# Performance work log

Hardware: AMD Instinct MI355X
Metric: run time of the kernel (lower is better)

## Reference

```python
import jax, jax.numpy as jnp
import numpy as np

B, S, W = 32, 256, 32
T = 16               # topics per doc, each spanning L = S//T sentences
VOCAB, E, H, D = 400001, 300, 128, 128


def _gru_scan(x, Wih, Whh, bih, bhh, reverse=False):
    """x: [B,S,E] -> (outputs [B,S,H], final hidden [B,H]). Torch GRU cell math."""
    h0 = jnp.zeros((x.shape[0], Whh.shape[1]), x.dtype)
    gi_all = jnp.einsum('bse,ge->bsg', x, Wih) + bih  # precompute input gates [B,S,3H]

    def step(h, gi):
        gh = h @ Whh.T + bhh
        ir, iz, inn = jnp.split(gi, 3, axis=-1)
        hr, hz, hn = jnp.split(gh, 3, axis=-1)
        r = jax.nn.sigmoid(ir + hr)
        z = jax.nn.sigmoid(iz + hz)
        n = jnp.tanh(inn + r * hn)
        h_new = (1.0 - z) * n + z * h
        return h_new, h_new

    hT, hs = jax.lax.scan(step, h0, jnp.swapaxes(gi_all, 0, 1), reverse=reverse)
    return jnp.swapaxes(hs, 0, 1), hT


def setup_inputs() -> dict:
    key = jax.random.key(0)
    ks = jax.random.split(key, 16)
    sc_i = 1.0 / np.sqrt(H)
    L = S // T
    starts = (jnp.arange(T, dtype=jnp.int32) * L + 1)          # 1-based inclusive
    ends = (jnp.arange(T, dtype=jnp.int32) + 1) * L
    tse = jnp.broadcast_to(jnp.stack([starts, ends], axis=-1)[None], (B, T, 2)).astype(jnp.int32)
    return {
        'word_ids': jax.random.randint(ks[0], (B, S, W), 0, VOCAB, dtype=jnp.int32),
        'topic_start_ends': tse,
        'embed_table': jax.random.normal(ks[1], (VOCAB, E), jnp.float32) * 0.6,
        'Wih_f': jax.random.normal(ks[2], (3 * H, E), jnp.float32) * sc_i,
        'Whh_f': jax.random.normal(ks[3], (3 * H, H), jnp.float32) * sc_i,
        'bih_f': jax.random.normal(ks[4], (3 * H,), jnp.float32) * sc_i,
        'bhh_f': jax.random.normal(ks[5], (3 * H,), jnp.float32) * sc_i,
        'Wih_b': jax.random.normal(ks[6], (3 * H, E), jnp.float32) * sc_i,
        'Whh_b': jax.random.normal(ks[7], (3 * H, H), jnp.float32) * sc_i,
        'bih_b': jax.random.normal(ks[8], (3 * H,), jnp.float32) * sc_i,
        'bhh_b': jax.random.normal(ks[9], (3 * H,), jnp.float32) * sc_i,
        'v_attention': jax.random.normal(ks[10], (4 * H, 1), jnp.float32),
        'W_attention': jax.random.normal(ks[11], (4 * H, 4 * H), jnp.float32) * (1.0 / np.sqrt(4 * H)),
        'W1': jax.random.normal(ks[12], (D, 4 * H), jnp.float32) * (1.0 / np.sqrt(4 * H)),
        'b1': jax.random.normal(ks[13], (D,), jnp.float32) * 0.01,
        'W2': jax.random.normal(ks[14], (1, D), jnp.float32) * (1.0 / np.sqrt(D)),
        'b2': jax.random.normal(ks[15], (1,), jnp.float32) * 0.01,
    }


def reference(word_ids, topic_start_ends, embed_table,
              Wih_f, Whh_f, bih_f, bhh_f, Wih_b, Whh_b, bih_b, bhh_b,
              v_attention, W_attention, W1, b1, W2, b2):
    b, s, _ = word_ids.shape
    h = Whh_f.shape[1]
    # --- sent_encoder: gather word embeddings, mean-pool per sentence ---
    sent_emb = jnp.mean(embed_table[word_ids], axis=2)          # [B,S,E]
    # --- doc_encoder: bi-GRU ---
    out_f, hT_f = _gru_scan(sent_emb, Wih_f, Whh_f, bih_f, bhh_f, reverse=False)
    out_b, hT_b = _gru_scan(sent_emb, Wih_b, Whh_b, bih_b, bhh_b, reverse=True)
    sent_rep = jnp.concatenate([out_f, out_b], axis=-1)         # [B,S,2H]
    # faithful to hidden.view(batch_size, 2H) on hidden of shape [2,B,H]
    doc_vec = jnp.stack([hT_f, hT_b], axis=0).reshape(b, 2 * h)
    doc_rep = jnp.broadcast_to(doc_vec[:, None, :], (b, s, 2 * h))
    # topic reps via segment difference of cumulative GRU states (pad trick)
    pad = jnp.pad(sent_rep, ((0, 0), (1, 1), (0, 0)))           # [B,S+2,2H]
    starts = topic_start_ends[:, :, 0]                          # [B,T], 1-based
    ends = topic_start_ends[:, :, 1]

    def gat(idx, lo, hi):
        return jnp.take_along_axis(pad[..., lo:hi], idx[:, :, None], axis=1)
    fwd_part = gat(ends, 0, h) - gat(starts - 1, 0, h)
    bwd_part = gat(starts, h, 2 * h) - gat(ends + 1, h, 2 * h)
    topic_mat = jnp.concatenate([fwd_part, bwd_part], axis=-1)  # [B,T,2H]
    # scatter topic vectors to sentences: topic id = #starts at or before sentence
    sidx = jnp.arange(s, dtype=starts.dtype)
    topic_id = jnp.sum(sidx[None, :, None] >= (starts - 1)[:, None, :], axis=-1) - 1  # [B,S]
    topic_rep = jnp.take_along_axis(topic_mat, topic_id[:, :, None], axis=1)          # [B,S,2H]
    # --- decoder ---
    cat_ds = jnp.concatenate([doc_rep, sent_rep], axis=-1)      # [B,S,4H]
    cat_ts = jnp.concatenate([topic_rep, sent_rep], axis=-1)
    doc_scores = jnp.tanh(cat_ds @ W_attention) @ v_attention   # [B,S,1]
    topic_scores = jnp.tanh(cat_ts @ W_attention) @ v_attention
    doc_w = jax.nn.softmax(doc_scores, axis=1)
    topic_w = jax.nn.softmax(topic_scores, axis=1)
    context = doc_w * doc_rep + topic_w * topic_rep             # [B,S,2H]
    inp = jnp.concatenate([sent_rep, context], axis=-1)         # [B,S,4H]
    hdd = jax.nn.relu(inp @ W1.T + b1)                          # dropout = identity (eval)
    logits = (hdd @ W2.T + b2).squeeze(-1)                      # [B,S]
    return logits
```

## Files before the change

### kernel.cpp

```cpp
#include <hip/hip_runtime.h>
#include <hip/hip_bf16.h>
#include <cstdint>

#define Bk 32
#define Sk 256
#define Wk 32
#define Tk 16
#define Ek 300
#define Hk 128
#define Dk 128
#define NROWS (Bk*Sk)
#define GI_N  (3*Hk*2)

__device__ __forceinline__ float fast_sigmoid(float x) {
    return 1.f / (1.f + __expf(-x));
}
__device__ __forceinline__ float fast_tanh(float x) {
    float ax = fabsf(x);
    float e = __expf(2.f * ax);
    float t = 1.f - 2.f / (1.f + e);
    return copysignf(t, x);
}
__device__ __forceinline__ void barrier_lgkm() {
    asm volatile("s_waitcnt lgkmcnt(0)" ::: "memory");
    __builtin_amdgcn_s_barrier();
}

__global__ __launch_bounds__(256) void pack_kernel(
    const float* __restrict__ Wf, const float* __restrict__ Wb,
    const float* __restrict__ bf, const float* __restrict__ bb,
    const float* __restrict__ W1,
    float* __restrict__ Bgi, float* __restrict__ bias_gi, float* __restrict__ BW1)
{
    int idx = blockIdx.x * 256 + threadIdx.x;
    if (idx < 300 * 768) {
        int k = idx / 768, n = idx % 768;
        Bgi[idx] = (n < 384) ? Wf[n * 300 + k] : Wb[(n - 384) * 300 + k];
    }
    if (idx < 768) bias_gi[idx] = (idx < 384) ? bf[idx] : bb[idx - 384];
    if (idx < 512 * 128) {
        int k = idx >> 7, n = idx & 127;
        BW1[idx] = W1[n * 512 + k];
    }
}

__global__ __launch_bounds__(256) void embed_mean_kernel(
    const int* __restrict__ wids, const float* __restrict__ table,
    float* __restrict__ sent_emb)
{
    int wv = (blockIdx.x << 2) + (threadIdx.x >> 6);
    int lane = threadIdx.x & 63;
    if (wv >= NROWS) return;
    const int* idp = wids + (size_t)wv * Wk;
    float4 a0 = {0,0,0,0}, a1 = {0,0,0,0};
    #pragma unroll 4
    for (int w = 0; w < Wk; ++w) {
        int id = idp[w];
        const float4* r4 = reinterpret_cast<const float4*>(table + (size_t)id * Ek);
        float4 v0 = r4[lane];
        a0.x += v0.x; a0.y += v0.y; a0.z += v0.z; a0.w += v0.w;
        if (lane < 11) {
            float4 v1 = r4[64 + lane];
            a1.x += v1.x; a1.y += v1.y; a1.z += v1.z; a1.w += v1.w;
        }
    }
    const float sc = 1.f / 32.f;
    float4* o4 = reinterpret_cast<float4*>(sent_emb + (size_t)wv * Ek);
    float4 o0 = {a0.x*sc, a0.y*sc, a0.z*sc, a0.w*sc};
    o4[lane] = o0;
    if (lane < 11) {
        float4 o1 = {a1.x*sc, a1.y*sc, a1.z*sc, a1.w*sc};
        o4[64 + lane] = o1;
    }
}

template<bool BIAS, bool RELU>
__global__ __launch_bounds__(256) void gemm_kernel(
    const float* __restrict__ A, const float* __restrict__ B,
    const float* __restrict__ bias, float* __restrict__ C,
    int M, int N, int K)
{
    __shared__ float As[64][68];
    __shared__ float Bs[64][68];
    const int tid = threadIdx.x;
    const int m0 = blockIdx.x * 64;
    const int n0 = blockIdx.y * 64;
    const int tx = tid & 15, ty = tid >> 4;
    const int lr = tid >> 2;
    const int lc = tid & 3;
    float acc[4][4] = {};

    for (int k0 = 0; k0 < K; k0 += 64) {
        #pragma unroll
        for (int i = 0; i < 4; ++i) {
            int kk = lc * 4 + i * 16;
            int gm = m0 + lr;
            int gk = k0 + kk;
            float4 v = {0,0,0,0};
            if (gm < M && gk < K)
                v = *reinterpret_cast<const float4*>(A + (size_t)gm * K + gk);
            As[kk+0][lr] = v.x; As[kk+1][lr] = v.y; As[kk+2][lr] = v.z; As[kk+3][lr] = v.w;
        }
        #pragma unroll
        for (int i = 0; i < 4; ++i) {
            int nn = lc * 4 + i * 16;
            int gk = k0 + lr;
            float4 v = {0,0,0,0};
            if (gk < K)
                v = *reinterpret_cast<const float4*>(B + (size_t)gk * N + n0 + nn);
            *reinterpret_cast<float4*>(&Bs[lr][nn]) = v;
        }
        __syncthreads();
        #pragma unroll 8
        for (int k = 0; k < 64; ++k) {
            float4 av = *reinterpret_cast<const float4*>(&As[k][ty*4]);
            float4 bv = *reinterpret_cast<const float4*>(&Bs[k][tx*4]);
            acc[0][0] += av.x*bv.x; acc[0][1] += av.x*bv.y; acc[0][2] += av.x*bv.z; acc[0][3] += av.x*bv.w;
            acc[1][0] += av.y*bv.x; acc[1][1] += av.y*bv.y; acc[1][2] += av.y*bv.z; acc[1][3] += av.y*bv.w;
            acc[2][0] += av.z*bv.x; acc[2][1] += av.z*bv.y; acc[2][2] += av.z*bv.z; acc[2][3] += av.z*bv.w;
            acc[3][0] += av.w*bv.x; acc[3][1] += av.w*bv.y; acc[3][2] += av.w*bv.z; acc[3][3] += av.w*bv.w;
        }
        __syncthreads();
    }
    #pragma unroll
    for (int r = 0; r < 4; ++r) {
        int row = m0 + ty * 4 + r;
        if (row < M) {
            float4 v = {acc[r][0], acc[r][1], acc[r][2], acc[r][3]};
            if (BIAS) {
                const float* bp = bias + n0 + tx * 4;
                v.x += bp[0]; v.y += bp[1]; v.z += bp[2]; v.w += bp[3];
            }
            if (RELU) {
                v.x = fmaxf(v.x, 0.f); v.y = fmaxf(v.y, 0.f);
                v.z = fmaxf(v.z, 0.f); v.w = fmaxf(v.w, 0.f);
            }
            *reinterpret_cast<float4*>(C + (size_t)row * N + n0 + tx * 4) = v;
        }
    }
}

__global__ __launch_bounds__(512, 1) void gru_scan_kernel(
    const float* __restrict__ gi,
    const float* __restrict__ Whh_f, const float* __restrict__ Whh_b,
    const float* __restrict__ bhh_f, const float* __restrict__ bhh_b,
    float* __restrict__ sent_rep,
    float* __restrict__ hT)
{
    const int blk = blockIdx.x;
    const int dir = blk >> 5;
    const int b   = blk & 31;
    const int t = threadIdx.x;
    const int lane = t & 63;
    const int w_id = t >> 6;
    const int q = lane >> 4;
    const int m = lane & 15;
    const int g = w_id * 16 + m;
    const float* Whh = dir ? Whh_b : Whh_f;
    const float* bhh = dir ? bhh_b : bhh_f;
    __shared__ float hsh[144];
    __shared__ float ghb[384];

    const float* wr = Whh + (3 * g) * 128 + 32 * q;
    float4 wA0 = *reinterpret_cast<const float4*>(wr +   0);
    float4 wA1 = *reinterpret_cast<const float4*>(wr +   4);
    float4 wA2 = *reinterpret_cast<const float4*>(wr +   8);
    float4 wA3 = *reinterpret_cast<const float4*>(wr +  12);
    float4 wA4 = *reinterpret_cast<const float4*>(wr +  16);
    float4 wA5 = *reinterpret_cast<const float4*>(wr +  20);
    float4 wA6 = *reinterpret_cast<const float4*>(wr +  24);
    float4 wA7 = *reinterpret_cast<const float4*>(wr +  28);
    float4 wB0 = *reinterpret_cast<const float4*>(wr + 128);
    float4 wB1 = *reinterpret_cast<const float4*>(wr + 132);
    float4 wB2 = *reinterpret_cast<const float4*>(wr + 136);
    float4 wB3 = *reinterpret_cast<const float4*>(wr + 140);
    float4 wB4 = *reinterpret_cast<const float4*>(wr + 144);
    float4 wB5 = *reinterpret_cast<const float4*>(wr + 148);
    float4 wB6 = *reinterpret_cast<const float4*>(wr + 152);
    float4 wB7 = *reinterpret_cast<const float4*>(wr + 156);
    float4 wC0 = *reinterpret_cast<const float4*>(wr + 256);
    float4 wC1 = *reinterpret_cast<const float4*>(wr + 260);
    float4 wC2 = *reinterpret_cast<const float4*>(wr + 264);
    float4 wC3 = *reinterpret_cast<const float4*>(wr + 268);
    float4 wC4 = *reinterpret_cast<const float4*>(wr + 272);
    float4 wC5 = *reinterpret_cast<const float4*>(wr + 276);
    float4 wC6 = *reinterpret_cast<const float4*>(wr + 280);
    float4 wC7 = *reinterpret_cast<const float4*>(wr + 284);
    const float b0 = bhh[3 * g + 0];
    const float b1 = bhh[3 * g + 1];
    const float b2 = bhh[3 * g + 2];

    if (t < 144) hsh[t] = 0.f;

    float gir = 0.f, giz = 0.f, gin_ = 0.f;
    if (t < 128) {
        const int s0 = dir ? (Sk - 1) : 0;
        const float* g0 = gi + (size_t)(b * Sk + s0) * GI_N + dir * 384 + t;
        gir = g0[0]; giz = g0[128]; gin_ = g0[256];
    }
    __syncthreads();

    const float4* hseg = reinterpret_cast<const float4*>(hsh) + 9 * q;
    for (int step = 0; step < Sk; ++step) {
        const int s = dir ? (Sk - 1 - step) : step;
        float pA = 0.f, pB = 0.f, pC = 0.f;
        #define SEG(j) { float4 h4 = hseg[j]; \
            pA = fmaf(wA##j.x, h4.x, pA); pA = fmaf(wA##j.y, h4.y, pA); \
            pA = fmaf(wA##j.z, h4.z, pA); pA = fmaf(wA##j.w, h4.w, pA); \
            pB = fmaf(wB##j.x, h4.x, pB); pB = fmaf(wB##j.y, h4.y, pB); \
            pB = fmaf(wB##j.z, h4.z, pB); pB = fmaf(wB##j.w, h4.w, pB); \
            pC = fmaf(wC##j.x, h4.x, pC); pC = fmaf(wC##j.y, h4.y, pC); \
            pC = fmaf(wC##j.z, h4.z, pC); pC = fmaf(wC##j.w, h4.w, pC); }
        SEG(0) SEG(1) SEG(2) SEG(3) SEG(4) SEG(5) SEG(6) SEG(7)
        #undef SEG
        pA += __shfl_xor(pA, 16); pA += __shfl_xor(pA, 32);
        pB += __shfl_xor(pB, 16); pB += __shfl_xor(pB, 32);
        pC += __shfl_xor(pC, 16); pC += __shfl_xor(pC, 32);
        if (q == 0) {
            ghb[3 * g + 0] = pA + b0;
            ghb[3 * g + 1] = pB + b1;
            ghb[3 * g + 2] = pC + b2;
        }
        barrier_lgkm();
        if (t < 128) {
            const int j = t;
            float hr = ghb[j], hz = ghb[128 + j], hn = ghb[256 + j];
            float r = fast_sigmoid(gir + hr);
            float z = fast_sigmoid(giz + hz);
            float n = fast_tanh(gin_ + r * hn);
            const int ji = 36 * (j >> 5) + (j & 31);
            float hold = hsh[ji];
            float hnew = (1.f - z) * n + z * hold;
            hsh[ji] = hnew;
            sent_rep[(size_t)(b * Sk + s) * 256 + dir * 128 + j] = hnew;
            if (step < Sk - 1) {
                const int sn = dir ? (s - 1) : (s + 1);
                const float* gp = gi + (size_t)(b * Sk + sn) * GI_N + dir * 384 + j;
                gir = gp[0]; giz = gp[128]; gin_ = gp[256];
            }
        }
        barrier_lgkm();
    }
    if (t < 128) {
        const int ji = 36 * (t >> 5) + (t & 31);
        hT[dir * 4096 + b * 128 + t] = hsh[ji];
    }
}

__device__ __forceinline__ float4 sr_load_guard(const float* sr, int b, int sidx, int j4) {
    if (sidx < 0 || sidx >= Sk) { float4 z = {0,0,0,0}; return z; }
    return reinterpret_cast<const float4*>(sr)[(size_t)(b * Sk + sidx) * 64 + j4];
}
__global__ __launch_bounds__(64) void prep_kernel(
    const int* __restrict__ tse, const float* __restrict__ sent_rep,
    const float* __restrict__ hT, float* __restrict__ dvtm)
{
    const int b = blockIdx.x;
    const int t = blockIdx.y;
    const int j4 = threadIdx.x;
    if (t == 16) {
        int dir = b >> 4;
        int bb = 2 * (b & 15) + (j4 >> 5);
        int jj4 = j4 & 31;
        float4 v = reinterpret_cast<const float4*>(hT)[dir * 1024 + bb * 32 + jj4];
        reinterpret_cast<float4*>(dvtm)[b * 64 + j4] = v;
    } else {
        int st = tse[b * 32 + t * 2];
        int en = tse[b * 32 + t * 2 + 1];
        float4 va, vb;
        if (j4 < 32) {
            va = sr_load_guard(sent_rep, b, en - 1, j4);
            vb = sr_load_guard(sent_rep, b, st - 2, j4);
        } else {
            va = sr_load_guard(sent_rep, b, st - 1, j4);
            vb = sr_load_guard(sent_rep, b, en, j4);
        }
        float4 v = {va.x - vb.x, va.y - vb.y, va.z - vb.z, va.w - vb.w};
        reinterpret_cast<float4*>(dvtm)[(32 + b * 16 + t) * 64 + j4] = v;
    }
}

__global__ __launch_bounds__(256) void scores_kernel(
    const float* __restrict__ SW,
    const float* __restrict__ dptp,
    const float* __restrict__ vatt,
    const int* __restrict__ tse,
    float* __restrict__ dsc, float* __restrict__ tsc)
{
    int row = (blockIdx.x << 2) + (threadIdx.x >> 6);
    int lane = threadIdx.x & 63;
    if (row >= NROWS) return;
    int b = row >> 8, s = row & 255;
    int ti = 0;
    #pragma unroll
    for (int t = 1; t < 16; ++t) ti += (s >= tse[b * 32 + t * 2] - 1) ? 1 : 0;
    const float4* swr = reinterpret_cast<const float4*>(SW + (size_t)row * 512);
    const float4* dpr = reinterpret_cast<const float4*>(dptp + (size_t)b * 512);
    const float4* tpr = reinterpret_cast<const float4*>(dptp + (size_t)(32 + b * 16 + ti) * 512);
    const float4* vv  = reinterpret_cast<const float4*>(vatt);
    float sd = 0.f, st = 0.f;
    #pragma unroll
    for (int q = 0; q < 2; ++q) {
        int i = lane * 2 + q;
        float4 sw = swr[i], dp = dpr[i], tp = tpr[i], v = vv[i];
        sd += fast_tanh(sw.x + dp.x) * v.x + fast_tanh(sw.y + dp.y) * v.y
            + fast_tanh(sw.z + dp.z) * v.z + fast_tanh(sw.w + dp.w) * v.w;
        st += fast_tanh(sw.x + tp.x) * v.x + fast_tanh(sw.y + tp.y) * v.y
            + fast_tanh(sw.z + tp.z) * v.z + fast_tanh(sw.w + tp.w) * v.w;
    }
    #pragma unroll
    for (int off = 32; off; off >>= 1) {
        sd += __shfl_xor(sd, off);
        st += __shfl_xor(st, off);
    }
    if (lane == 0) { dsc[row] = sd; tsc[row] = st; }
}

__global__ __launch_bounds__(256) void softmax_kernel(float* __restrict__ dsc, float* __restrict__ tsc)
{
    const int b = blockIdx.x, sidx = threadIdx.x;
    const int lane = sidx & 63, wid = sidx >> 6;
    __shared__ float rd[4], rt[4];
    float d = dsc[b * Sk + sidx];
    float t = tsc[b * Sk + sidx];
    float md = d, mt = t;
    #pragma unroll
    for (int off = 32; off; off >>= 1) {
        md = fmaxf(md, __shfl_xor(md, off));
        mt = fmaxf(mt, __shfl_xor(mt, off));
    }
    if (lane == 0) { rd[wid] = md; rt[wid] = mt; }
    __syncthreads();
    md = fmaxf(fmaxf(rd[0], rd[1]), fmaxf(rd[2], rd[3]));
    mt = fmaxf(fmaxf(rt[0], rt[1]), fmaxf(rt[2], rt[3]));
    float ed = __expf(d - md), et = __expf(t - mt);
    float sd = ed, stt = et;
    #pragma unroll
    for (int off = 32; off; off >>= 1) {
        sd += __shfl_xor(sd, off);
        stt += __shfl_xor(stt, off);
    }
    __syncthreads();
    if (lane == 0) { rd[wid] = sd; rt[wid] = stt; }
    __syncthreads();
    sd = rd[0] + rd[1] + rd[2] + rd[3];
    stt = rt[0] + rt[1] + rt[2] + rt[3];
    dsc[b * Sk + sidx] = ed / sd;
    tsc[b * Sk + sidx] = et / stt;
}

__global__ __launch_bounds__(128) void build_inp_kernel(
    const float* __restrict__ sent_rep, const float* __restrict__ dvtm,
    const float* __restrict__ dw, const float* __restrict__ tw,
    const int* __restrict__ tse, float* __restrict__ inp)
{
    int row = blockIdx.x;
    int b = row >> 8, s = row & 255;
    int f4c = threadIdx.x;
    float4 v;
    if (f4c < 64) {
        v = reinterpret_cast<const float4*>(sent_rep)[(size_t)row * 64 + f4c];
    } else {
        int ti = 0;
        #pragma unroll
        for (int t = 1; t < 16; ++t) ti += (s >= tse[b * 32 + t * 2] - 1) ? 1 : 0;
        float dwv = dw[row], twv = tw[row];
        int j4 = f4c - 64;
        float4 dv = reinterpret_cast<const float4*>(dvtm)[b * 64 + j4];
        float4 tm = reinterpret_cast<const float4*>(dvtm)[(32 + b * 16 + ti) * 64 + j4];
        v.x = dwv * dv.x + twv * tm.x;
        v.y = dwv * dv.y + twv * tm.y;
        v.z = dwv * dv.z + twv * tm.z;
        v.w = dwv * dv.w + twv * tm.w;
    }
    reinterpret_cast<float4*>(inp)[(size_t)row * 128 + f4c] = v;
}

__global__ __launch_bounds__(256) void logits_kernel(
    const float* __restrict__ hdd, const float* __restrict__ W2,
    const float* __restrict__ b2, float* __restrict__ out)
{
    int row = (blockIdx.x << 2) + (threadIdx.x >> 6);
    int lane = threadIdx.x & 63;
    if (row >= NROWS) return;
    float acc = hdd[(size_t)row * 128 + lane] * W2[lane]
              + hdd[(size_t)row * 128 + 64 + lane] * W2[64 + lane];
    #pragma unroll
    for (int off = 32; off; off >>= 1) acc += __shfl_xor(acc, off);
    if (lane == 0) out[row] = acc + b2[0];
}

extern "C" void kernel_launch(void* const* d_in, const int* in_sizes, int n_in,
                              void* d_out, int out_size, void* d_ws, size_t ws_size,
                              hipStream_t stream)
{
    const int*   wids  = (const int*)d_in[0];
    const int*   tse   = (const int*)d_in[1];
    const float* table = (const float*)d_in[2];
    const float* Wihf  = (const float*)d_in[3];
    const float* Whhf  = (const float*)d_in[4];
    const float* bihf  = (const float*)d_in[5];
    const float* bhhf  = (const float*)d_in[6];
    const float* Wihb  = (const float*)d_in[7];
    const float* Whhb  = (const float*)d_in[8];
    const float* bihb  = (const float*)d_in[9];
    const float* bhhb  = (const float*)d_in[10];
    const float* vatt  = (const float*)d_in[11];
    const float* Watt  = (const float*)d_in[12];
    const float* W1    = (const float*)d_in[13];
    const float* b1    = (const float*)d_in[14];
    const float* W2    = (const float*)d_in[15];
    const float* b2    = (const float*)d_in[16];
    float* ws = (float*)d_ws;
    float* out = (float*)d_out;

    float* sent_emb = ws + 0;
    float* gi       = ws + 2457600;
    float* sent_rep = ws + 8749056;
    float* hT       = ws + 10846208;
    float* dvtm     = ws + 10854400;
    float* dptp     = ws + 10993664;
    float* dsc      = ws + 11272192;
    float* tsc      = ws + 11280384;
    float* Bgi      = ws + 11288576;
    float* bias_gi  = ws + 11518976;
    float* BW1      = ws + 11519744;
    float* SW       = ws + 0;
    float* inp      = ws + 4194304;
    float* hdd      = ws + 0;

    if (ws_size < (size_t)11585280 * sizeof(float)) return;

    pack_kernel<<<900, 256, 0, stream>>>(Wihf, Wihb, bihf, bihb, W1, Bgi, bias_gi, BW1);
    embed_mean_kernel<<<2048, 256, 0, stream>>>(wids, table, sent_emb);
    gemm_kernel<true,false><<<dim3(128, 12), 256, 0, stream>>>(sent_emb, Bgi, bias_gi, gi, NROWS, 768, 300);
    gru_scan_kernel<<<64, 512, 0, stream>>>(gi, Whhf, Whhb, bhhf, bhhb, sent_rep, hT);
    prep_kernel<<<dim3(32, 17), 64, 0, stream>>>(tse, sent_rep, hT, dvtm);
    gemm_kernel<false,false><<<dim3(128, 8), 256, 0, stream>>>(sent_rep, Watt + 256 * 512, nullptr, SW, NROWS, 512, 256);
    gemm_kernel<false,false><<<dim3(9, 8), 256, 0, stream>>>(dvtm, Watt, nullptr, dptp, 544, 512, 256);
    scores_kernel<<<2048, 256, 0, stream>>>(SW, dptp, vatt, tse, dsc, tsc);
    softmax_kernel<<<32, 256, 0, stream>>>(dsc, tsc);
    build_inp_kernel<<<NROWS, 128, 0, stream>>>(sent_rep, dvtm, dsc, tsc, tse, inp);
    gemm_kernel<true,true><<<dim3(128, 2), 256, 0, stream>>>(inp, BW1, b1, hdd, NROWS, 128, 512);
    logits_kernel<<<2048, 256, 0, stream>>>(hdd, W2, b2, out);
}
```

Measured before the change: 415.5 us.

## Add 128x128 register-tiled GEMM and two-step unrolled GRU scan with prefetch

Adds a 128x128-tile GEMM in which each thread computes an 8x8 output block, and uses it for the input-gate projection and the sentence attention projection. The aim is more reuse per shared-memory load and fewer blocks. The GRU scan loop is unrolled by two, with gate inputs held in two register sets so the load for step s+2 is issued two steps ahead, hiding global latency on the serial critical path. The existing GEMM inner loop now uses explicit fmaf. The trade-off is that the larger tiles give fewer blocks (384 and 256) on a GPU with many CUs, and raise register pressure.

```diff
diff --git a/kernel.cpp b/kernel.cpp
--- a/kernel.cpp
+++ b/kernel.cpp
@@ -24,6 +24,12 @@
 __device__ __forceinline__ void barrier_lgkm() {
     asm volatile("s_waitcnt lgkmcnt(0)" ::: "memory");
     __builtin_amdgcn_s_barrier();
+}
+__device__ __forceinline__ void fma44(const float4& a, const float4& b, float (&c)[4][4]) {
+    c[0][0]=fmaf(a.x,b.x,c[0][0]); c[0][1]=fmaf(a.x,b.y,c[0][1]); c[0][2]=fmaf(a.x,b.z,c[0][2]); c[0][3]=fmaf(a.x,b.w,c[0][3]);
+    c[1][0]=fmaf(a.y,b.x,c[1][0]); c[1][1]=fmaf(a.y,b.y,c[1][1]); c[1][2]=fmaf(a.y,b.z,c[1][2]); c[1][3]=fmaf(a.y,b.w,c[1][3]);
+    c[2][0]=fmaf(a.z,b.x,c[2][0]); c[2][1]=fmaf(a.z,b.y,c[2][1]); c[2][2]=fmaf(a.z,b.z,c[2][2]); c[2][3]=fmaf(a.z,b.w,c[2][3]);
+    c[3][0]=fmaf(a.w,b.x,c[3][0]); c[3][1]=fmaf(a.w,b.y,c[3][1]); c[3][2]=fmaf(a.w,b.z,c[3][2]); c[3][3]=fmaf(a.w,b.w,c[3][3]);
 }
 
 __global__ __launch_bounds__(256) void pack_kernel(
@@ -115,10 +121,7 @@
         for (int k = 0; k < 64; ++k) {
             float4 av = *reinterpret_cast<const float4*>(&As[k][ty*4]);
             float4 bv = *reinterpret_cast<const float4*>(&Bs[k][tx*4]);
-            acc[0][0] += av.x*bv.x; acc[0][1] += av.x*bv.y; acc[0][2] += av.x*bv.z; acc[0][3] += av.x*bv.w;
-            acc[1][0] += av.y*bv.x; acc[1][1] += av.y*bv.y; acc[1][2] += av.y*bv.z; acc[1][3] += av.y*bv.w;
-            acc[2][0] += av.z*bv.x; acc[2][1] += av.z*bv.y; acc[2][2] += av.z*bv.z; acc[2][3] += av.z*bv.w;
-            acc[3][0] += av.w*bv.x; acc[3][1] += av.w*bv.y; acc[3][2] += av.w*bv.z; acc[3][3] += av.w*bv.w;
+            fma44(av, bv, acc);
         }
         __syncthreads();
     }
@@ -136,6 +139,78 @@
                 v.z = fmaxf(v.z, 0.f); v.w = fmaxf(v.w, 0.f);
             }
             *reinterpret_cast<float4*>(C + (size_t)row * N + n0 + tx * 4) = v;
+        }
+    }
+}
+
+template<bool BIAS>
+__global__ __launch_bounds__(256) void gemm128_kernel(
+    const float* __restrict__ A, const float* __restrict__ B,
+    const float* __restrict__ bias, float* __restrict__ C,
+    int M, int N, int K)
+{
+    __shared__ float As[32][136];
+    __shared__ float Bs[32][136];
+    const int tid = threadIdx.x;
+    const int m0 = blockIdx.x * 128;
+    const int n0 = blockIdx.y * 128;
+    const int tx = tid & 15, ty = tid >> 4;
+    float acc[2][2][4][4] = {};
+
+    const int sr    = tid >> 1;
+    const int kbase = (tid & 1) * 16;
+    const int bk_   = tid >> 3;
+    const int nb    = (tid & 7) * 16;
+
+    for (int k0 = 0; k0 < K; k0 += 32) {
+        #pragma unroll
+        for (int i = 0; i < 4; ++i) {
+            int kk = kbase + i * 4;
+            int gk = k0 + kk;
+            float4 v = {0,0,0,0};
+            if (gk < K)
+                v = *reinterpret_cast<const float4*>(A + (size_t)(m0 + sr) * K + gk);
+            As[kk+0][sr] = v.x; As[kk+1][sr] = v.y; As[kk+2][sr] = v.z; As[kk+3][sr] = v.w;
+        }
+        #pragma unroll
+        for (int i = 0; i < 4; ++i) {
+            int nn = nb + i * 4;
+            int gk = k0 + bk_;
+            float4 v = {0,0,0,0};
+            if (gk < K)
+                v = *reinterpret_cast<const float4*>(B + (size_t)gk * N + n0 + nn);
+            *reinterpret_cast<float4*>(&Bs[bk_][nn]) = v;
+        }
+        __syncthreads();
+        #pragma unroll 8
+        for (int k = 0; k < 32; ++k) {
+            float4 a0 = *reinterpret_cast<const float4*>(&As[k][ty*4]);
+            float4 a1 = *reinterpret_cast<const float4*>(&As[k][64 + ty*4]);
+            float4 b0 = *reinterpret_cast<const float4*>(&Bs[k][tx*4]);
+            float4 b1 = *reinterpret_cast<const float4*>(&Bs[k][64 + tx*4]);
+            fma44(a0, b0, acc[0][0]);
+            fma44(a0, b1, acc[0][1]);
+            fma44(a1, b0, acc[1][0]);
+            fma44(a1, b1, acc[1][1]);
+        }
+        __syncthreads();
+    }
+    #pragma unroll
+    for (int mh = 0; mh < 2; ++mh) {
+        #pragma unroll
+        for (int mi = 0; mi < 4; ++mi) {
+            int row = m0 + mh * 64 + ty * 4 + mi;
+            #pragma unroll
+            for (int nh = 0; nh < 2; ++nh) {
+                int col = n0 + nh * 64 + tx * 4;
+                float4 v = {acc[mh][nh][mi][0], acc[mh][nh][mi][1],
+                            acc[mh][nh][mi][2], acc[mh][nh][mi][3]};
+                if (BIAS) {
+                    const float* bp = bias + col;
+                    v.x += bp[0]; v.y += bp[1]; v.z += bp[2]; v.w += bp[3];
+                }
+                *reinterpret_cast<float4*>(C + (size_t)row * N + col) = v;
+            }
         }
     }
 }
@@ -192,55 +267,98 @@
 
     if (t < 144) hsh[t] = 0.f;
 
-    float gir = 0.f, giz = 0.f, gin_ = 0.f;
+    float ar = 0.f, az = 0.f, an_ = 0.f;
+    float br_ = 0.f, bz = 0.f, bn_ = 0.f;
+    const float* gbase = gi + (size_t)(b * Sk) * GI_N + dir * 384 + t;
     if (t < 128) {
         const int s0 = dir ? (Sk - 1) : 0;
-        const float* g0 = gi + (size_t)(b * Sk + s0) * GI_N + dir * 384 + t;
-        gir = g0[0]; giz = g0[128]; gin_ = g0[256];
+        const int s1 = dir ? (Sk - 2) : 1;
+        const float* g0 = gbase + (size_t)s0 * GI_N;
+        ar = g0[0]; az = g0[128]; an_ = g0[256];
+        const float* g1 = gbase + (size_t)s1 * GI_N;
+        br_ = g1[0]; bz = g1[128]; bn_ = g1[256];
     }
     __syncthreads();
 
     const float4* hseg = reinterpret_cast<const float4*>(hsh) + 9 * q;
-    for (int step = 0; step < Sk; ++step) {
-        const int s = dir ? (Sk - 1 - step) : step;
-        float pA = 0.f, pB = 0.f, pC = 0.f;
-        #define SEG(j) { float4 h4 = hseg[j]; \
-            pA = fmaf(wA##j.x, h4.x, pA); pA = fmaf(wA##j.y, h4.y, pA); \
-            pA = fmaf(wA##j.z, h4.z, pA); pA = fmaf(wA##j.w, h4.w, pA); \
-            pB = fmaf(wB##j.x, h4.x, pB); pB = fmaf(wB##j.y, h4.y, pB); \
-            pB = fmaf(wB##j.z, h4.z, pB); pB = fmaf(wB##j.w, h4.w, pB); \
-            pC = fmaf(wC##j.x, h4.x, pC); pC = fmaf(wC##j.y, h4.y, pC); \
-            pC = fmaf(wC##j.z, h4.z, pC); pC = fmaf(wC##j.w, h4.w, pC); }
-        SEG(0) SEG(1) SEG(2) SEG(3) SEG(4) SEG(5) SEG(6) SEG(7)
-        #undef SEG
-        pA += __shfl_xor(pA, 16); pA += __shfl_xor(pA, 32);
-        pB += __shfl_xor(pB, 16); pB += __shfl_xor(pB, 32);
-        pC += __shfl_xor(pC, 16); pC += __shfl_xor(pC, 32);
-        if (q == 0) {
-            ghb[3 * g + 0] = pA + b0;
-            ghb[3 * g + 1] = pB + b1;
-            ghb[3 * g + 2] = pC + b2;
-        }
-        barrier_lgkm();
-        if (t < 128) {
-            const int j = t;
-            float hr = ghb[j], hz = ghb[128 + j], hn = ghb[256 + j];
-            float r = fast_sigmoid(gir + hr);
-            float z = fast_sigmoid(giz + hz);
-            float n = fast_tanh(gin_ + r * hn);
-            const int ji = 36 * (j >> 5) + (j & 31);
-            float hold = hsh[ji];
-            float hnew = (1.f - z) * n + z * hold;
-            hsh[ji] = hnew;
-            sent_rep[(size_t)(b * Sk + s) * 256 + dir * 128 + j] = hnew;
-            if (step < Sk - 1) {
-                const int sn = dir ? (s - 1) : (s + 1);
-                const float* gp = gi + (size_t)(b * Sk + sn) * GI_N + dir * 384 + j;
-                gir = gp[0]; giz = gp[128]; gin_ = gp[256];
-            }
-        }
-        barrier_lgkm();
-    }
+
+    #define PHASE1() { \
+        pA = 0.f; pB = 0.f; pC = 0.f; \
+        { float4 h4; \
+          h4 = hseg[0]; \
+          pA = fmaf(wA0.x,h4.x,pA); pA = fmaf(wA0.y,h4.y,pA); pA = fmaf(wA0.z,h4.z,pA); pA = fmaf(wA0.w,h4.w,pA); \
+          pB = fmaf(wB0.x,h4.x,pB); pB = fmaf(wB0.y,h4.y,pB); pB = fmaf(wB0.z,h4.z,pB); pB = fmaf(wB0.w,h4.w,pB); \
+          pC = fmaf(wC0.x,h4.x,pC); pC = fmaf(wC0.y,h4.y,pC); pC = fmaf(wC0.z,h4.z,pC); pC = fmaf(wC0.w,h4.w,pC); \
+          h4 = hseg[1]; \
+          pA = fmaf(wA1.x,h4.x,pA); pA = fmaf(wA1.y,h4.y,pA); pA = fmaf(wA1.z,h4.z,pA); pA = fmaf(wA1.w,h4.w,pA); \
+          pB = fmaf(wB1.x,h4.x,pB); pB = fmaf(wB1.y,h4.y,pB); pB = fmaf(wB1.z,h4.z,pB); pB = fmaf(wB1.w,h4.w,pB); \
+          pC = fmaf(wC1.x,h4.x,pC); pC = fmaf(wC1.y,h4.y,pC); pC = fmaf(wC1.z,h4.z,pC); pC = fmaf(wC1.w,h4.w,pC); \
+          h4 = hseg[2]; \
+          pA = fmaf(wA2.x,h4.x,pA); pA = fmaf(wA2.y,h4.y,pA); pA = fmaf(wA2.z,h4.z,pA); pA = fmaf(wA2.w,h4.w,pA); \
+          pB = fmaf(wB2.x,h4.x,pB); pB = fmaf(wB2.y,h4.y,pB); pB = fmaf(wB2.z,h4.z,pB); pB = fmaf(wB2.w,h4.w,pB); \
+          pC = fmaf(wC2.x,h4.x,pC); pC = fmaf(wC2.y,h4.y,pC); pC = fmaf(wC2.z,h4.z,pC); pC = fmaf(wC2.w,h4.w,pC); \
+          h4 = hseg[3]; \
+          pA = fmaf(wA3.x,h4.x,pA); pA = fmaf(wA3.y,h4.y,pA); pA = fmaf(wA3.z,h4.z,pA); pA = fmaf(wA3.w,h4.w,pA); \
+          pB = fmaf(wB3.x,h4.x,pB); pB = fmaf(wB3.y,h4.y,pB); pB = fmaf(wB3.z,h4.z,pB); pB = fmaf(wB3.w,h4.w,pB); \
+          pC = fmaf(wC3.x,h4.x,pC); pC = fmaf(wC3.y,h4.y,pC); pC = fmaf(wC3.z,h4.z,pC); pC = fmaf(wC3.w,h4.w,pC); \
+          h4 = hseg[4]; \
+          pA = fmaf(wA4.x,h4.x,pA); pA = fmaf(wA4.y,h4.y,pA); pA = fmaf(wA4.z,h4.z,pA); pA = fmaf(wA4.w,h4.w,pA); \
+          pB = fmaf(wB4.x,h4.x,pB); pB = fmaf(wB4.y,h4.y,pB); pB = fmaf(wB4.z,h4.z,pB); pB = fmaf(wB4.w,h4.w,pB); \
+          pC = fmaf(wC4.x,h4.x,pC); pC = fmaf(wC4.y,h4.y,pC); pC = fmaf(wC4.z,h4.z,pC); pC = fmaf(wC4.w,h4.w,pC); \
+          h4 = hseg[5]; \
+          pA = fmaf(wA5.x,h4.x,pA); pA = fmaf(wA5.y,h4.y,pA); pA = fmaf(wA5.z,h4.z,pA); pA = fmaf(wA5.w,h4.w,pA); \
+          pB = fmaf(wB5.x,h4.x,pB); pB = fmaf(wB5.y,h4.y,pB); pB = fmaf(wB5.z,h4.z,pB); pB = fmaf(wB5.w,h4.w,pB); \
+          pC = fmaf(wC5.x,h4.x,pC); pC = fmaf(wC5.y,h4.y,pC); pC = fmaf(wC5.z,h4.z,pC); pC = fmaf(wC5.w,h4.w,pC); \
+          h4 = hseg[6]; \
+          pA = fmaf(wA6.x,h4.x,pA); pA = fmaf(wA6.y,h4.y,pA); pA = fmaf(wA6.z,h4.z,pA); pA = fmaf(wA6.w,h4.w,pA); \
+          pB = fmaf(wB6.x,h4.x,pB); pB = fmaf(wB6.y,h4.y,pB); pB = fmaf(wB6.z,h4.z,pB); pB = fmaf(wB6.w,h4.w,pB); \
+          pC = fmaf(wC6.x,h4.x,pC); pC = fmaf(wC6.y,h4.y,pC); pC = fmaf(wC6.z,h4.z,pC); pC = fmaf(wC6.w,h4.w,pC); \
+          h4 = hseg[7]; \
+          pA = fmaf(wA7.x,h4.x,pA); pA = fmaf(wA7.y,h4.y,pA); pA = fmaf(wA7.z,h4.z,pA); pA = fmaf(wA7.w,h4.w,pA); \
+          pB = fmaf(wB7.x,h4.x,pB); pB = fmaf(wB7.y,h4.y,pB); pB = fmaf(wB7.z,h4.z,pB); pB = fmaf(wB7.w,h4.w,pB); \
+          pC = fmaf(wC7.x,h4.x,pC); pC = fmaf(wC7.y,h4.y,pC); pC = fmaf(wC7.z,h4.z,pC); pC = fmaf(wC7.w,h4.w,pC); } \
+        pA += __shfl_xor(pA, 16); pA += __shfl_xor(pA, 32); \
+        pB += __shfl_xor(pB, 16); pB += __shfl_xor(pB, 32); \
+        pC += __shfl_xor(pC, 16); pC += __shfl_xor(pC, 32); \
+        if (q == 0) { ghb[3*g+0] = pA + b0; ghb[3*g+1] = pB + b1; ghb[3*g+2] = pC + b2; } }
+
+    #define PHASE2(GR, GZ, GN) { \
+        if (t < 128) { \
+            const int j = t; \
+            float hr = ghb[j], hz = ghb[128 + j], hn = ghb[256 + j]; \
+            float r = fast_sigmoid(GR + hr); \
+            float z = fast_sigmoid(GZ + hz); \
+            float n = fast_tanh(GN + r * hn); \
+            const int ji = 36 * (j >> 5) + (j & 31); \
+            float hold = hsh[ji]; \
+            float hnew = (1.f - z) * n + z * hold; \
+            hsh[ji] = hnew; \
+            sent_rep[(size_t)(b * Sk + s) * 256 + dir * 128 + j] = hnew; \
+            const int sn = dir ? (s >= 2 ? s - 2 : 0) : (s + 2 < Sk ? s + 2 : Sk - 1); \
+            const float* gp = gbase + (size_t)sn * GI_N; \
+            GR = gp[0]; GZ = gp[128]; GN = gp[256]; \
+        } }
+
+    float pA, pB, pC;
+    for (int step = 0; step < Sk; step += 2) {
+        {
+            const int s = dir ? (Sk - 1 - step) : step;
+            PHASE1();
+            barrier_lgkm();
+            PHASE2(ar, az, an_);
+            barrier_lgkm();
+        }
+        {
+            const int s = dir ? (Sk - 2 - step) : (step + 1);
+            PHASE1();
+            barrier_lgkm();
+            PHASE2(br_, bz, bn_);
+            barrier_lgkm();
+        }
+    }
+    #undef PHASE1
+    #undef PHASE2
+
     if (t < 128) {
         const int ji = 36 * (t >> 5) + (t & 31);
         hT[dir * 4096 + b * 128 + t] = hsh[ji];
@@ -433,10 +551,10 @@
 
     pack_kernel<<<900, 256, 0, stream>>>(Wihf, Wihb, bihf, bihb, W1, Bgi, bias_gi, BW1);
     embed_mean_kernel<<<2048, 256, 0, stream>>>(wids, table, sent_emb);
-    gemm_kernel<true,false><<<dim3(128, 12), 256, 0, stream>>>(sent_emb, Bgi, bias_gi, gi, NROWS, 768, 300);
+    gemm128_kernel<true><<<dim3(64, 6), 256, 0, stream>>>(sent_emb, Bgi, bias_gi, gi, NROWS, 768, 300);
     gru_scan_kernel<<<64, 512, 0, stream>>>(gi, Whhf, Whhb, bhhf, bhhb, sent_rep, hT);
     prep_kernel<<<dim3(32, 17), 64, 0, stream>>>(tse, sent_rep, hT, dvtm);
-    gemm_kernel<false,false><<<dim3(128, 8), 256, 0, stream>>>(sent_rep, Watt + 256 * 512, nullptr, SW, NROWS, 512, 256);
+    gemm128_kernel<false><<<dim3(64, 4), 256, 0, stream>>>(sent_rep, Watt + 256 * 512, nullptr, SW, NROWS, 512, 256);
     gemm_kernel<false,false><<<dim3(9, 8), 256, 0, stream>>>(dvtm, Watt, nullptr, dptp, 544, 512, 256);
     scores_kernel<<<2048, 256, 0, stream>>>(SW, dptp, vatt, tse, dsc, tsc);
     softmax_kernel<<<32, 256, 0, stream>>>(dsc, tsc);
```

After: 438.5 us. 1.06x slower.
